# Kernel optimization log

Measured on AMD Instinct MI355X. Metric: run time of the kernel, lower is better.

## Reference

```python
import jax, jax.numpy as jnp
import numpy as np

B, T, D, H = 2, 2048, 1024, 16
DK = D // H


def setup_inputs() -> dict:
    key = jax.random.key(0)
    ks = jax.random.split(key, 12)
    q = jax.random.normal(ks[0], (B, T, D), jnp.float32)
    k = jax.random.normal(ks[1], (B, T, D), jnp.float32)
    v = jax.random.normal(ks[2], (B, T, D), jnp.float32)
    # padding mask [B,1,T]: 1 = valid, 0 = pad (nonzero per torch eq(0) semantics)
    lengths = jnp.array([T, (3 * T) // 4])
    mask = (jnp.arange(T)[None, None, :] < lengths[:, None, None]).astype(jnp.int32)
    s = 0.02
    Wq = jax.random.normal(ks[3], (D, D), jnp.float32) * s
    Wk = jax.random.normal(ks[4], (D, D), jnp.float32) * s
    Wv = jax.random.normal(ks[5], (D, D), jnp.float32) * s
    Wo = jax.random.normal(ks[6], (D, D), jnp.float32) * s
    bq = jnp.zeros((D,), jnp.float32)
    bk = jnp.zeros((D,), jnp.float32)
    bv = jnp.zeros((D,), jnp.float32)
    bo = jnp.zeros((D,), jnp.float32)
    return {"query": q, "key": k, "value": v, "mask": mask,
            "Wq": Wq, "bq": bq, "Wk": Wk, "bk": bk,
            "Wv": Wv, "bv": bv, "Wo": Wo, "bo": bo}


def reference(query, key, value, mask, Wq, bq, Wk, bk, Wv, bv, Wo, bo):
    # q,k,v projections -> [B, H, T, DK]
    def proj(x, W, b):
        return (x @ W.T + b).reshape(B, T, H, DK).transpose(0, 2, 1, 3)
    q = proj(query, Wq, bq)
    k = proj(key, Wk, bk)
    v = proj(value, Wv, bv)
    scores = jnp.einsum("bhqd,bhkd->bhqk", q, k) * (DK ** -0.5)  # [B,H,T,T]
    m = (mask == 0)[:, None, :, :]  # [B,1,1,T] broadcast over heads/queries
    scores = jnp.where(m, -jnp.inf, scores)
    attn = jax.nn.softmax(scores, axis=-1)
    attn = jnp.where(m, 0.0, attn)
    x = jnp.einsum("bhqk,bhkd->bhqd", attn, v)  # [B,H,T,DK]
    x = x.transpose(0, 2, 1, 3).reshape(B, T, D)
    return x @ Wo.T + bo
```

## Files before the change

### kernel.cpp

```cpp
#include <hip/hip_runtime.h>

typedef unsigned short u16;
typedef unsigned int u32;
typedef __bf16 bf16x8 __attribute__((ext_vector_type(8)));
typedef float floatx4 __attribute__((ext_vector_type(4)));

#define BB 2
#define TT 2048
#define DD 1024
#define HH 16
#define DKK 64
#define ACT (BB * TT * DD)
#define WTE (DD * DD)

__device__ inline u16 f2bf(float f) {
    union { float f; u32 u; } c; c.f = f;
    u32 r = (c.u + 0x7fffu + ((c.u >> 16) & 1u)) >> 16;
    return (u16)r;
}
__device__ inline u32 pack2bf(float a, float b) {
    return (u32)f2bf(a) | ((u32)f2bf(b) << 16);
}

typedef __attribute__((address_space(1))) const u32 gas_u32;
typedef __attribute__((address_space(3))) u32 las_u32;
__device__ __forceinline__ void gl2lds16(const u16* g, u16* l) {
    __builtin_amdgcn_global_load_lds((gas_u32*)g, (las_u32*)l, 16, 0, 0);
}

__device__ __forceinline__ u32 cvtpk_bf16(float lo, float hi) {
    u32 r;
    asm("v_cvt_pk_bf16_f32 %0, %1, %2" : "=v"(r) : "v"(lo), "v"(hi));
    return r;
}

__device__ __forceinline__ void quad_gather(u32 &a, u32 &b) {
    asm volatile("s_nop 1\n\t"
                 "v_permlane32_swap_b32 %0, %1\n\t"
                 "s_nop 1\n\t"
                 "v_permlane16_swap_b32 %0, %1"
                 : "+v"(a), "+v"(b));
}

struct CvtArgs { const float* src[7]; u16* dst[7]; };
__global__ __launch_bounds__(256) void convert_bf16(CvtArgs a) {
    int bid = blockIdx.x, t, local;
    if (bid < 768) { t = bid >> 8; local = bid & 255; }
    else { int r = bid - 768; t = 3 + (r >> 6); local = r & 63; }
    const float* s = a.src[t];
    u16* d = a.dst[t];
    const int base = local * 16384;
    for (int i = 0; i < 8; i++) {
        const int idx = base + i * 2048 + threadIdx.x * 8;
        float4 x0 = *(const float4*)(s + idx);
        float4 x1 = *(const float4*)(s + idx + 4);
        uint4 p;
        p.x = pack2bf(x0.x, x0.y); p.y = pack2bf(x0.z, x0.w);
        p.z = pack2bf(x1.x, x1.y); p.w = pack2bf(x1.z, x1.w);
        *(uint4*)(d + idx) = p;
    }
}

__global__ __launch_bounds__(256) void qkv_gemm(
    const u16* __restrict__ Qc, const u16* __restrict__ Kc,
    const u16* __restrict__ Vc,
    const u16* __restrict__ Wqc, const u16* __restrict__ Wkc,
    const u16* __restrict__ Wvc,
    const float* __restrict__ bq, const float* __restrict__ bk,
    const float* __restrict__ bv,
    u16* __restrict__ ws)
{
    __shared__ __align__(16) u16 As[128 * 32];
    __shared__ __align__(16) u16 Bs[128 * 32];
    const int l = (blockIdx.x & 7) * 96 + (blockIdx.x >> 3);
    const int z = l >> 8;
    const int yy = (l & 255) >> 3;
    const int xx = l & 7;
    const u16* A = (z == 0) ? Qc : (z == 1) ? Kc : Vc;
    const u16* W = (z == 0) ? Wqc : (z == 1) ? Wkc : Wvc;
    const float* bias = (z == 0) ? bq : (z == 1) ? bk : bv;
    u16* out = ws + (size_t)z * (size_t)BB * HH * TT * DKK;

    const int tid  = threadIdx.x;
    const int wave = tid >> 6, lane = tid & 63;
    const int quad = lane >> 4, l16 = lane & 15;
    const int wm = wave & 1, wn = wave >> 1;
    const int m0 = yy * 128, n0 = xx * 128;
    const int K = DD;

    const int lrow = lane >> 2, lcol = (lane & 3) * 8;
    const u16* Ag0 = A + (size_t)(m0 + wave * 16 + lrow) * K + lcol;
    const u16* Ag1 = A + (size_t)(m0 + 64 + wave * 16 + lrow) * K + lcol;
    const u16* Wg0 = W + (size_t)(n0 + wave * 16 + lrow) * K + lcol;
    const u16* Wg1 = W + (size_t)(n0 + 64 + wave * 16 + lrow) * K + lcol;
    u16* AsD0 = &As[(wave * 16) * 32];
    u16* AsD1 = &As[(64 + wave * 16) * 32];
    u16* BsD0 = &Bs[(wave * 16) * 32];
    u16* BsD1 = &Bs[(64 + wave * 16) * 32];

    floatx4 acc[4][4];
    for (int i = 0; i < 4; i++)
        for (int j = 0; j < 4; j++)
            acc[i][j] = floatx4{0.f, 0.f, 0.f, 0.f};

    for (int k0 = 0; k0 < K; k0 += 32) {
        __syncthreads();
        gl2lds16(Ag0 + k0, AsD0);
        gl2lds16(Ag1 + k0, AsD1);
        gl2lds16(Wg0 + k0, BsD0);
        gl2lds16(Wg1 + k0, BsD1);
        __syncthreads();

        bf16x8 af[4], bfr[4];
        for (int mi = 0; mi < 4; mi++)
            af[mi] = *(const bf16x8*)&As[(wm * 64 + mi * 16 + l16) * 32 + quad * 8];
        for (int ni = 0; ni < 4; ni++)
            bfr[ni] = *(const bf16x8*)&Bs[(wn * 64 + ni * 16 + l16) * 32 + quad * 8];
        for (int mi = 0; mi < 4; mi++)
            for (int ni = 0; ni < 4; ni++)
                acc[mi][ni] = __builtin_amdgcn_mfma_f32_16x16x32_bf16(
                    af[mi], bfr[ni], acc[mi][ni], 0, 0, 0);
    }

    for (int ni = 0; ni < 4; ni++) {
        const int n = n0 + wn * 64 + ni * 16 + l16;
        const float bv2 = bias[n];
        const int h = n >> 6, dk = n & 63;
        for (int mi = 0; mi < 4; mi++) {
            if (z == 2) {
                const int m = m0 + wm * 64 + mi * 16 + quad * 4;
                const int b = m >> 11, t = m & 2047;
                uint2 pp;
                pp.x = pack2bf(acc[mi][ni][0] + bv2, acc[mi][ni][1] + bv2);
                pp.y = pack2bf(acc[mi][ni][2] + bv2, acc[mi][ni][3] + bv2);
                *(uint2*)&out[(((size_t)(b * HH + h)) * DKK + dk) * TT + t] = pp;
            } else {
                for (int vv = 0; vv < 4; vv++) {
                    const int m = m0 + wm * 64 + mi * 16 + quad * 4 + vv;
                    const int b = m >> 11, t = m & 2047;
                    out[(((size_t)(b * HH + h)) * TT + t) * DKK + dk] =
                        f2bf(acc[mi][ni][vv] + bv2);
                }
            }
        }
    }
}

__global__ __launch_bounds__(256) void out_gemm(
    const u16* __restrict__ Av, const u16* __restrict__ Wv,
    const float* __restrict__ bias, float* __restrict__ outv)
{
    __shared__ __align__(16) u16 As[128 * 32];
    __shared__ __align__(16) u16 Bs[128 * 32];
    const int l = (blockIdx.x & 7) * 32 + (blockIdx.x >> 3);
    const int yy = l >> 3, xx = l & 7;
    const int tid  = threadIdx.x;
    const int wave = tid >> 6, lane = tid & 63;
    const int quad = lane >> 4, l16 = lane & 15;
    const int wm = wave & 1, wn = wave >> 1;
    const int m0 = yy * 128, n0 = xx * 128;
    const int K = DD, N = DD;

    const int lrow = lane >> 2, lcol = (lane & 3) * 8;
    const u16* Ag0 = Av + (size_t)(m0 + wave * 16 + lrow) * K + lcol;
    const u16* Ag1 = Av + (size_t)(m0 + 64 + wave * 16 + lrow) * K + lcol;
    const u16* Wg0 = Wv + (size_t)(n0 + wave * 16 + lrow) * K + lcol;
    const u16* Wg1 = Wv + (size_t)(n0 + 64 + wave * 16 + lrow) * K + lcol;
    u16* AsD0 = &As[(wave * 16) * 32];
    u16* AsD1 = &As[(64 + wave * 16) * 32];
    u16* BsD0 = &Bs[(wave * 16) * 32];
    u16* BsD1 = &Bs[(64 + wave * 16) * 32];

    floatx4 acc[4][4];
    for (int i = 0; i < 4; i++)
        for (int j = 0; j < 4; j++)
            acc[i][j] = floatx4{0.f, 0.f, 0.f, 0.f};

    for (int k0 = 0; k0 < K; k0 += 32) {
        __syncthreads();
        gl2lds16(Ag0 + k0, AsD0);
        gl2lds16(Ag1 + k0, AsD1);
        gl2lds16(Wg0 + k0, BsD0);
        gl2lds16(Wg1 + k0, BsD1);
        __syncthreads();

        bf16x8 af[4], bfr[4];
        for (int mi = 0; mi < 4; mi++)
            af[mi] = *(const bf16x8*)&As[(wm * 64 + mi * 16 + l16) * 32 + quad * 8];
        for (int ni = 0; ni < 4; ni++)
            bfr[ni] = *(const bf16x8*)&Bs[(wn * 64 + ni * 16 + l16) * 32 + quad * 8];
        for (int mi = 0; mi < 4; mi++)
            for (int ni = 0; ni < 4; ni++)
                acc[mi][ni] = __builtin_amdgcn_mfma_f32_16x16x32_bf16(
                    af[mi], bfr[ni], acc[mi][ni], 0, 0, 0);
    }

    for (int ni = 0; ni < 4; ni++) {
        const int n = n0 + wn * 64 + ni * 16 + l16;
        const float bv2 = bias[n];
        for (int mi = 0; mi < 4; mi++)
            for (int vv = 0; vv < 4; vv++) {
                const int m = m0 + wm * 64 + mi * 16 + quad * 4 + vv;
                outv[(size_t)m * N + n] = acc[mi][ni][vv] + bv2;
            }
    }
}

__global__ __launch_bounds__(512) void attn_kernel(
    const u16* __restrict__ Qp, const u16* __restrict__ Kp,
    const u16* __restrict__ Vpt, const int* __restrict__ mask,
    u16* __restrict__ Xa)
{
    __shared__ __align__(16) u16 Ks[64 * 64];
    __shared__ __align__(16) u16 Vs[64 * 64];
    const int tid  = threadIdx.x;
    const int wave = tid >> 6, lane = tid & 63;
    const int quad = lane >> 4, l16 = lane & 15;
    const int bid = blockIdx.x;
    const int qt = bid & 15, bh = bid >> 4;
    const int b = bh >> 4, h = bh & 15;
    const int qbase = qt * 128 + wave * 16;

    const u16* Qb = Qp + (size_t)bh * TT * DKK;
    const u16* Kb = Kp + (size_t)bh * TT * DKK;
    const u16* Vb = Vpt + (size_t)bh * DKK * TT;
    const int* mk = mask + b * TT;

    const int srow = tid >> 3, sg = tid & 7;
    const int sgs = sg ^ (srow & 7);
    const u16* Ksrc = Kb + (size_t)srow * DKK + sgs * 8;
    const u16* Vsrc = Vb + (size_t)srow * TT + sgs * 8;
    u16* KsD = &Ks[srow * 64 + sg * 8];
    u16* VsD = &Vs[srow * 64 + sg * 8];

    const int x7 = l16 & 7;
    const int rg0 = (quad ^ x7) * 8;
    const int rg1 = ((quad + 4) ^ x7) * 8;

    const bf16x8 qf0 = *(const bf16x8*)&Qb[(size_t)(qbase + l16) * DKK + quad * 8];
    const bf16x8 qf1 = *(const bf16x8*)&Qb[(size_t)(qbase + l16) * DKK + 32 + quad * 8];

    floatx4 o[4];
    for (int i = 0; i < 4; i++) o[i] = floatx4{0.f, 0.f, 0.f, 0.f};
    float rs = 0.f;

    uint4 kr = *(const uint4*)Ksrc;
    uint4 vr = *(const uint4*)Vsrc;

    for (int ti = 0; ti < TT / 64; ti++) {
        const int k0 = ti * 64;
        __syncthreads();
        *(uint4*)KsD = kr;
        *(uint4*)VsD = vr;
        __syncthreads();
        if (ti + 1 < TT / 64) {
            kr = *(const uint4*)(Ksrc + (size_t)(k0 + 64) * DKK);
            vr = *(const uint4*)(Vsrc + (k0 + 64));
        }

        const int mv0 = mk[k0 + l16];
        const int mv1 = mk[k0 + 16 + l16];
        const int mv2 = mk[k0 + 32 + l16];
        const int mv3 = mk[k0 + 48 + l16];
        if (!__any(mv0 | mv1 | mv2 | mv3)) continue;
        const bool allv = __all(mv0 && mv1 && mv2 && mv3);

        bf16x8 kf[4][2];
        #pragma unroll
        for (int c = 0; c < 4; c++) {
            const u16* kb = &Ks[(c * 16 + l16) * 64];
            kf[c][0] = *(const bf16x8*)&kb[rg0];
            kf[c][1] = *(const bf16x8*)&kb[rg1];
        }

        floatx4 s[4];
        #pragma unroll
        for (int c = 0; c < 4; c++) s[c] = floatx4{0.f, 0.f, 0.f, 0.f};
        #pragma unroll
        for (int c = 0; c < 4; c++) {
            s[c] = __builtin_amdgcn_mfma_f32_16x16x32_bf16(kf[c][0], qf0, s[c], 0, 0, 0);
            s[c] = __builtin_amdgcn_mfma_f32_16x16x32_bf16(kf[c][1], qf1, s[c], 0, 0, 0);
        }

        float p[4][4];
        if (allv) {
            #pragma unroll
            for (int c = 0; c < 4; c++)
                #pragma unroll
                for (int v = 0; v < 4; v++)
                    p[c][v] = __expf(s[c][v] * 0.125f);
        } else {
            #pragma unroll
            for (int c = 0; c < 4; c++)
                #pragma unroll
                for (int v = 0; v < 4; v++)
                    p[c][v] = mk[k0 + c * 16 + quad * 4 + v]
                                  ? __expf(s[c][v] * 0.125f) : 0.f;
        }
        #pragma unroll
        for (int c = 0; c < 4; c++)
            #pragma unroll
            for (int v = 0; v < 4; v++)
                rs += p[c][v];

        u32 A0 = cvtpk_bf16(p[0][0], p[0][1]), B0 = cvtpk_bf16(p[1][0], p[1][1]);
        u32 A1 = cvtpk_bf16(p[0][2], p[0][3]), B1 = cvtpk_bf16(p[1][2], p[1][3]);
        u32 A2 = cvtpk_bf16(p[2][0], p[2][1]), B2 = cvtpk_bf16(p[3][0], p[3][1]);
        u32 A3 = cvtpk_bf16(p[2][2], p[2][3]), B3 = cvtpk_bf16(p[3][2], p[3][3]);
        quad_gather(A0, B0);
        quad_gather(A1, B1);
        quad_gather(A2, B2);
        quad_gather(A3, B3);
        union { u32 w[4]; bf16x8 v; } pa0, pa1;
        pa0.w[0] = A0; pa0.w[1] = A1; pa0.w[2] = B0; pa0.w[3] = B1;
        pa1.w[0] = A2; pa1.w[1] = A3; pa1.w[2] = B2; pa1.w[3] = B3;

        #pragma unroll
        for (int nb = 0; nb < 4; nb++) {
            const u16* vb = &Vs[(nb * 16 + l16) * 64];
            const bf16x8 vf0 = *(const bf16x8*)&vb[rg0];
            const bf16x8 vf1 = *(const bf16x8*)&vb[rg1];
            o[nb] = __builtin_amdgcn_mfma_f32_16x16x32_bf16(pa0.v, vf0, o[nb], 0, 0, 0);
            o[nb] = __builtin_amdgcn_mfma_f32_16x16x32_bf16(pa1.v, vf1, o[nb], 0, 0, 0);
        }
    }

    rs += __shfl_xor(rs, 16, 64);
    rs += __shfl_xor(rs, 32, 64);
    float inv[4];
    #pragma unroll
    for (int v = 0; v < 4; v++)
        inv[v] = 1.0f / __shfl(rs, quad * 4 + v, 64);

    #pragma unroll
    for (int nb = 0; nb < 4; nb++)
        #pragma unroll
        for (int v = 0; v < 4; v++) {
            const int t = qbase + quad * 4 + v;
            Xa[((size_t)b * TT + t) * DD + h * DKK + nb * 16 + l16] =
                f2bf(o[nb][v] * inv[v]);
        }
}

extern "C" void kernel_launch(void* const* d_in, const int* in_sizes, int n_in,
                              void* d_out, int out_size, void* d_ws, size_t ws_size,
                              hipStream_t stream) {
    const float* q    = (const float*)d_in[0];
    const float* k    = (const float*)d_in[1];
    const float* v    = (const float*)d_in[2];
    const int*   mask = (const int*)d_in[3];
    const float* Wq   = (const float*)d_in[4];
    const float* bq   = (const float*)d_in[5];
    const float* Wk   = (const float*)d_in[6];
    const float* bk   = (const float*)d_in[7];
    const float* Wv   = (const float*)d_in[8];
    const float* bv   = (const float*)d_in[9];
    const float* Wo   = (const float*)d_in[10];
    const float* bo   = (const float*)d_in[11];

    u16* Qc  = (u16*)d_ws;
    u16* Kc  = Qc + (size_t)ACT;
    u16* Vc  = Kc + (size_t)ACT;
    u16* Wqc = Vc + (size_t)ACT;
    u16* Wkc = Wqc + (size_t)WTE;
    u16* Wvc = Wkc + (size_t)WTE;
    u16* Woc = Wvc + (size_t)WTE;
    u16* Qp  = Woc + (size_t)WTE;
    u16* Kp  = Qp + (size_t)ACT;
    u16* Vpt = Kp + (size_t)ACT;
    u16* Xa  = Vpt + (size_t)ACT;

    CvtArgs ca;
    ca.src[0] = q;  ca.dst[0] = Qc;
    ca.src[1] = k;  ca.dst[1] = Kc;
    ca.src[2] = v;  ca.dst[2] = Vc;
    ca.src[3] = Wq; ca.dst[3] = Wqc;
    ca.src[4] = Wk; ca.dst[4] = Wkc;
    ca.src[5] = Wv; ca.dst[5] = Wvc;
    ca.src[6] = Wo; ca.dst[6] = Woc;
    convert_bf16<<<1024, 256, 0, stream>>>(ca);

    qkv_gemm<<<dim3(768), 256, 0, stream>>>(
        Qc, Kc, Vc, Wqc, Wkc, Wvc, bq, bk, bv, Qp);

    attn_kernel<<<dim3(BB * HH * (TT / 128)), 512, 0, stream>>>(Qp, Kp, Vpt, mask, Xa);

    out_gemm<<<dim3(256), 256, 0, stream>>>(Xa, Woc, bo, (float*)d_out);
}
```

Before: 234.3 us.

## Fuse fp32-to-bf16 activation conversion into QKV GEMM and halve out_gemm M tile

The separate conversion pass over the q/k/v activations is removed. The QKV GEMM now loads fp32 activation tiles into registers, converts them to bf16 with packed converts and stores them into LDS, prefetching the next K slice during compute. This avoids writing and re-reading three bf16 activation copies through global memory, at the cost of more register pressure and synchronous LDS stores in the GEMM loop. Separately, the output GEMM uses a 64-row M tile with twice as many blocks to improve occupancy and CU fill.

```diff
diff --git a/kernel.cpp b/kernel.cpp
--- a/kernel.cpp
+++ b/kernel.cpp
@@ -42,11 +42,9 @@
                  : "+v"(a), "+v"(b));
 }
 
-struct CvtArgs { const float* src[7]; u16* dst[7]; };
+struct CvtArgs { const float* src[4]; u16* dst[4]; };
 __global__ __launch_bounds__(256) void convert_bf16(CvtArgs a) {
-    int bid = blockIdx.x, t, local;
-    if (bid < 768) { t = bid >> 8; local = bid & 255; }
-    else { int r = bid - 768; t = 3 + (r >> 6); local = r & 63; }
+    const int t = blockIdx.x >> 6, local = blockIdx.x & 63;
     const float* s = a.src[t];
     u16* d = a.dst[t];
     const int base = local * 16384;
@@ -62,8 +60,8 @@
 }
 
 __global__ __launch_bounds__(256) void qkv_gemm(
-    const u16* __restrict__ Qc, const u16* __restrict__ Kc,
-    const u16* __restrict__ Vc,
+    const float* __restrict__ Qf, const float* __restrict__ Kf,
+    const float* __restrict__ Vf,
     const u16* __restrict__ Wqc, const u16* __restrict__ Wkc,
     const u16* __restrict__ Wvc,
     const float* __restrict__ bq, const float* __restrict__ bk,
@@ -76,7 +74,7 @@
     const int z = l >> 8;
     const int yy = (l & 255) >> 3;
     const int xx = l & 7;
-    const u16* A = (z == 0) ? Qc : (z == 1) ? Kc : Vc;
+    const float* A = (z == 0) ? Qf : (z == 1) ? Kf : Vf;
     const u16* W = (z == 0) ? Wqc : (z == 1) ? Wkc : Wvc;
     const float* bias = (z == 0) ? bq : (z == 1) ? bk : bv;
     u16* out = ws + (size_t)z * (size_t)BB * HH * TT * DKK;
@@ -88,13 +86,13 @@
     const int m0 = yy * 128, n0 = xx * 128;
     const int K = DD;
 
+    const int ar = tid >> 1, ah = tid & 1;
+    const float* Afp = A + (size_t)(m0 + ar) * K + ah * 16;
+    u16* AsW = &As[ar * 32 + ah * 16];
+
     const int lrow = lane >> 2, lcol = (lane & 3) * 8;
-    const u16* Ag0 = A + (size_t)(m0 + wave * 16 + lrow) * K + lcol;
-    const u16* Ag1 = A + (size_t)(m0 + 64 + wave * 16 + lrow) * K + lcol;
     const u16* Wg0 = W + (size_t)(n0 + wave * 16 + lrow) * K + lcol;
     const u16* Wg1 = W + (size_t)(n0 + 64 + wave * 16 + lrow) * K + lcol;
-    u16* AsD0 = &As[(wave * 16) * 32];
-    u16* AsD1 = &As[(64 + wave * 16) * 32];
     u16* BsD0 = &Bs[(wave * 16) * 32];
     u16* BsD1 = &Bs[(64 + wave * 16) * 32];
 
@@ -103,13 +101,31 @@
         for (int j = 0; j < 4; j++)
             acc[i][j] = floatx4{0.f, 0.f, 0.f, 0.f};
 
+    float4 areg[4];
+    #pragma unroll
+    for (int i = 0; i < 4; i++) areg[i] = *(const float4*)(Afp + i * 4);
+
     for (int k0 = 0; k0 < K; k0 += 32) {
         __syncthreads();
-        gl2lds16(Ag0 + k0, AsD0);
-        gl2lds16(Ag1 + k0, AsD1);
+        uint4 w0, w1;
+        w0.x = cvtpk_bf16(areg[0].x, areg[0].y);
+        w0.y = cvtpk_bf16(areg[0].z, areg[0].w);
+        w0.z = cvtpk_bf16(areg[1].x, areg[1].y);
+        w0.w = cvtpk_bf16(areg[1].z, areg[1].w);
+        w1.x = cvtpk_bf16(areg[2].x, areg[2].y);
+        w1.y = cvtpk_bf16(areg[2].z, areg[2].w);
+        w1.z = cvtpk_bf16(areg[3].x, areg[3].y);
+        w1.w = cvtpk_bf16(areg[3].z, areg[3].w);
+        *(uint4*)AsW = w0;
+        *(uint4*)(AsW + 8) = w1;
         gl2lds16(Wg0 + k0, BsD0);
         gl2lds16(Wg1 + k0, BsD1);
         __syncthreads();
+        if (k0 + 32 < K) {
+            #pragma unroll
+            for (int i = 0; i < 4; i++)
+                areg[i] = *(const float4*)(Afp + k0 + 32 + i * 4);
+        }
 
         bf16x8 af[4], bfr[4];
         for (int mi = 0; mi < 4; mi++)
@@ -150,46 +166,43 @@
     const u16* __restrict__ Av, const u16* __restrict__ Wv,
     const float* __restrict__ bias, float* __restrict__ outv)
 {
-    __shared__ __align__(16) u16 As[128 * 32];
+    __shared__ __align__(16) u16 As[64 * 32];
     __shared__ __align__(16) u16 Bs[128 * 32];
-    const int l = (blockIdx.x & 7) * 32 + (blockIdx.x >> 3);
+    const int l = (blockIdx.x & 7) * 64 + (blockIdx.x >> 3);
     const int yy = l >> 3, xx = l & 7;
     const int tid  = threadIdx.x;
     const int wave = tid >> 6, lane = tid & 63;
     const int quad = lane >> 4, l16 = lane & 15;
     const int wm = wave & 1, wn = wave >> 1;
-    const int m0 = yy * 128, n0 = xx * 128;
+    const int m0 = yy * 64, n0 = xx * 128;
     const int K = DD, N = DD;
 
     const int lrow = lane >> 2, lcol = (lane & 3) * 8;
     const u16* Ag0 = Av + (size_t)(m0 + wave * 16 + lrow) * K + lcol;
-    const u16* Ag1 = Av + (size_t)(m0 + 64 + wave * 16 + lrow) * K + lcol;
     const u16* Wg0 = Wv + (size_t)(n0 + wave * 16 + lrow) * K + lcol;
     const u16* Wg1 = Wv + (size_t)(n0 + 64 + wave * 16 + lrow) * K + lcol;
     u16* AsD0 = &As[(wave * 16) * 32];
-    u16* AsD1 = &As[(64 + wave * 16) * 32];
     u16* BsD0 = &Bs[(wave * 16) * 32];
     u16* BsD1 = &Bs[(64 + wave * 16) * 32];
 
-    floatx4 acc[4][4];
-    for (int i = 0; i < 4; i++)
+    floatx4 acc[2][4];
+    for (int i = 0; i < 2; i++)
         for (int j = 0; j < 4; j++)
             acc[i][j] = floatx4{0.f, 0.f, 0.f, 0.f};
 
     for (int k0 = 0; k0 < K; k0 += 32) {
         __syncthreads();
         gl2lds16(Ag0 + k0, AsD0);
-        gl2lds16(Ag1 + k0, AsD1);
         gl2lds16(Wg0 + k0, BsD0);
         gl2lds16(Wg1 + k0, BsD1);
         __syncthreads();
 
-        bf16x8 af[4], bfr[4];
-        for (int mi = 0; mi < 4; mi++)
-            af[mi] = *(const bf16x8*)&As[(wm * 64 + mi * 16 + l16) * 32 + quad * 8];
+        bf16x8 af[2], bfr[4];
+        for (int mi = 0; mi < 2; mi++)
+            af[mi] = *(const bf16x8*)&As[(wm * 32 + mi * 16 + l16) * 32 + quad * 8];
         for (int ni = 0; ni < 4; ni++)
             bfr[ni] = *(const bf16x8*)&Bs[(wn * 64 + ni * 16 + l16) * 32 + quad * 8];
-        for (int mi = 0; mi < 4; mi++)
+        for (int mi = 0; mi < 2; mi++)
             for (int ni = 0; ni < 4; ni++)
                 acc[mi][ni] = __builtin_amdgcn_mfma_f32_16x16x32_bf16(
                     af[mi], bfr[ni], acc[mi][ni], 0, 0, 0);
@@ -198,9 +211,9 @@
     for (int ni = 0; ni < 4; ni++) {
         const int n = n0 + wn * 64 + ni * 16 + l16;
         const float bv2 = bias[n];
-        for (int mi = 0; mi < 4; mi++)
+        for (int mi = 0; mi < 2; mi++)
             for (int vv = 0; vv < 4; vv++) {
-                const int m = m0 + wm * 64 + mi * 16 + quad * 4 + vv;
+                const int m = m0 + wm * 32 + mi * 16 + quad * 4 + vv;
                 outv[(size_t)m * N + n] = acc[mi][ni][vv] + bv2;
             }
     }
@@ -358,10 +371,7 @@
     const float* Wo   = (const float*)d_in[10];
     const float* bo   = (const float*)d_in[11];
 
-    u16* Qc  = (u16*)d_ws;
-    u16* Kc  = Qc + (size_t)ACT;
-    u16* Vc  = Kc + (size_t)ACT;
-    u16* Wqc = Vc + (size_t)ACT;
+    u16* Wqc = (u16*)d_ws;
     u16* Wkc = Wqc + (size_t)WTE;
     u16* Wvc = Wkc + (size_t)WTE;
     u16* Woc = Wvc + (size_t)WTE;
@@ -371,19 +381,16 @@
     u16* Xa  = Vpt + (size_t)ACT;
 
     CvtArgs ca;
-    ca.src[0] = q;  ca.dst[0] = Qc;
-    ca.src[1] = k;  ca.dst[1] = Kc;
-    ca.src[2] = v;  ca.dst[2] = Vc;
-    ca.src[3] = Wq; ca.dst[3] = Wqc;
-    ca.src[4] = Wk; ca.dst[4] = Wkc;
-    ca.src[5] = Wv; ca.dst[5] = Wvc;
-    ca.src[6] = Wo; ca.dst[6] = Woc;
-    convert_bf16<<<1024, 256, 0, stream>>>(ca);
+    ca.src[0] = Wq; ca.dst[0] = Wqc;
+    ca.src[1] = Wk; ca.dst[1] = Wkc;
+    ca.src[2] = Wv; ca.dst[2] = Wvc;
+    ca.src[3] = Wo; ca.dst[3] = Woc;
+    convert_bf16<<<256, 256, 0, stream>>>(ca);
 
     qkv_gemm<<<dim3(768), 256, 0, stream>>>(
-        Qc, Kc, Vc, Wqc, Wkc, Wvc, bq, bk, bv, Qp);
+        q, k, v, Wqc, Wkc, Wvc, bq, bk, bv, Qp);
 
     attn_kernel<<<dim3(BB * HH * (TT / 128)), 512, 0, stream>>>(Qp, Kp, Vpt, mask, Xa);
 
-    out_gemm<<<dim3(256), 256, 0, stream>>>(Xa, Woc, bo, (float*)d_out);
-}
+    out_gemm<<<dim3(512), 256, 0, stream>>>(Xa, Woc, bo, (float*)d_out);
+}
```

Result: slower. 255.8 us (+9.2%).
